# Performance work log

Measured on AMD Instinct MI355X. Metric: run time of the kernel, lower is better.

## Reference

```python
import jax, jax.numpy as jnp
import numpy as np

N_NODES = 100000
N_EDGES = 1600000
IN_CH, HID, EMB = 128, 64, 32


def _glorot(key, shape):
    lim = np.sqrt(6.0 / (shape[0] + shape[1])).astype(np.float32)
    return jax.random.uniform(key, shape, jnp.float32, -lim, lim)


def setup_inputs() -> dict:
    key = jax.random.key(0)
    ks = jax.random.split(key, 5)
    x = jax.random.normal(ks[0], (N_NODES, IN_CH), dtype=jnp.float32)
    edges = jax.random.randint(ks[1], (2, N_EDGES), 0, N_NODES)
    W1 = _glorot(ks[2], (IN_CH, HID)); b1 = jnp.zeros((HID,), jnp.float32)
    W2 = _glorot(ks[3], (HID, EMB)); b2 = jnp.zeros((EMB,), jnp.float32)
    W3 = _glorot(ks[4], (HID, EMB)); b3 = jnp.zeros((EMB,), jnp.float32)
    return {"x": x, "edges": edges, "W1": W1, "b1": b1,
            "W2": W2, "b2": b2, "W3": W3, "b3": b3}


def reference(x, edges, W1, b1, W2, b2, W3, b3):
    N = x.shape[0]
    # GCNConv default: add self-loops, symmetric D^-1/2 A D^-1/2 normalization
    loop = jnp.arange(N, dtype=edges.dtype)
    src = jnp.concatenate([edges[0], loop])  # [E+N] message sources
    dst = jnp.concatenate([edges[1], loop])  # [E+N] message targets
    deg = jax.ops.segment_sum(jnp.ones_like(dst, dtype=x.dtype), dst, num_segments=N)
    dinv = jnp.where(deg > 0, jax.lax.rsqrt(deg), 0.0)
    norm = dinv[src] * dinv[dst]  # [E+N], cached across the three convs (cached=True)

    def gcn(h, W, b):
        h = h @ W                                  # [N, out]
        msg = h[src] * norm[:, None]               # gather + edge scale
        return jax.ops.segment_sum(msg, dst, num_segments=N) + b  # scatter-add

    h = jax.nn.relu(gcn(x, W1, b1))
    return gcn(h, W2, b2), gcn(h, W3, b3)
```

## Files before the change

kernel.cpp:

```cpp
#include <hip/hip_runtime.h>

#define NN 100000
#define NE 1600000
#define NB 391
#define CHUNK 4096
#define NCHUNK 391

typedef __attribute__((ext_vector_type(8))) short short8_t;
typedef __attribute__((ext_vector_type(4))) float float4_t;

__device__ inline unsigned short f2bf(float f) {
    unsigned int u = __float_as_uint(f);
    unsigned int r = u + 0x7fffu + ((u >> 16) & 1u);
    return (unsigned short)(r >> 16);
}
__device__ inline float bf_lo(unsigned int u) { return __uint_as_float(u << 16); }
__device__ inline float bf_hi(unsigned int u) { return __uint_as_float(u & 0xffff0000u); }

__global__ __launch_bounds__(256) void k_hist(const int* __restrict__ dst,
                                              int* __restrict__ bhist) {
    __shared__ int lh[NB];
    int t = threadIdx.x;
    for (int i = t; i < NB; i += 256) lh[i] = 0;
    __syncthreads();
    for (int e = blockIdx.x * 256 + t; e < NE; e += 256 * 256)
        atomicAdd(&lh[dst[e] >> 8], 1);
    __syncthreads();
    for (int i = t; i < NB; i += 256)
        if (lh[i]) atomicAdd(&bhist[i], lh[i]);
}

__global__ __launch_bounds__(256) void k_scanb(const int* __restrict__ bhist,
                                               int* __restrict__ boff,
                                               int* __restrict__ bcur) {
    __shared__ int sh[256];
    int t = threadIdx.x;
    int base = t * 2;
    int v0 = (base + 0 < NB) ? bhist[base + 0] : 0;
    int v1 = (base + 1 < NB) ? bhist[base + 1] : 0;
    int tsum = v0 + v1;
    sh[t] = tsum;
    __syncthreads();
    for (int d = 1; d < 256; d <<= 1) {
        int x = (t >= d) ? sh[t - d] : 0;
        __syncthreads();
        sh[t] += x;
        __syncthreads();
    }
    int excl = sh[t] - tsum;
    if (base + 0 < NB) { boff[base + 0] = excl;      bcur[base + 0] = excl; }
    if (base + 1 < NB) { boff[base + 1] = excl + v0; bcur[base + 1] = excl + v0; }
    if (t == 255) boff[NB] = sh[255];
}

__global__ __launch_bounds__(512) void k_bscatter(const int* __restrict__ src,
                                                  const int* __restrict__ dst,
                                                  int* __restrict__ bcur,
                                                  unsigned int* __restrict__ pairs) {
    __shared__ int lh[NB];
    __shared__ int lbase[NB];
    int t = threadIdx.x;
    int e0 = blockIdx.x * CHUNK;
    int e1 = min(e0 + CHUNK, NE);
    for (int i = t; i < NB; i += 512) lh[i] = 0;
    __syncthreads();
    for (int e = e0 + t; e < e1; e += 512)
        atomicAdd(&lh[dst[e] >> 8], 1);
    __syncthreads();
    int rot = (int)((blockIdx.x * 97u) % NB);
    for (int i = t; i < NB; i += 512) {
        int ii = i + rot; if (ii >= NB) ii -= NB;
        int h = lh[ii];
        lbase[ii] = h ? atomicAdd(&bcur[ii], h) : 0;
    }
    __syncthreads();
    for (int i = t; i < NB; i += 512) lh[i] = 0;
    __syncthreads();
    for (int e = e0 + t; e < e1; e += 512) {
        int d = dst[e];
        int b = d >> 8;
        int r = atomicAdd(&lh[b], 1);
        pairs[lbase[b] + r] = (unsigned int)src[e] | ((unsigned int)(d & 255) << 17);
    }
}

__global__ __launch_bounds__(256) void k_fine(const unsigned int* __restrict__ pairs,
                                              const int* __restrict__ boff,
                                              int* __restrict__ csr_off,
                                              int* __restrict__ csr_src,
                                              float* __restrict__ dinv) {
    __shared__ int lcnt[256];
    __shared__ int sc[256];
    __shared__ int lofs[256];
    int t = threadIdx.x;
    int b = blockIdx.x;
    int n0 = b << 8;
    int nnode = min(256, NN - n0);
    int bO = boff[b], bE = boff[b + 1];

    lcnt[t] = 0;
    __syncthreads();
    for (int e = bO + t; e < bE; e += 256)
        atomicAdd(&lcnt[pairs[e] >> 17], 1);
    __syncthreads();
    sc[t] = lcnt[t];
    __syncthreads();
    for (int d = 1; d < 256; d <<= 1) {
        int x = (t >= d) ? sc[t - d] : 0;
        __syncthreads();
        sc[t] += x;
        __syncthreads();
    }
    {
        int excl = sc[t] - lcnt[t];
        lofs[t] = excl;
        if (t < nnode) {
            int n = n0 + t;
            csr_off[n] = bO + excl;
            dinv[n] = rsqrtf(1.0f + (float)lcnt[t]);
        }
        lcnt[t] = 0;
    }
    if (b == NB - 1 && t == 0) csr_off[NN] = NE;
    __syncthreads();
    for (int e = bO + t; e < bE; e += 256) {
        unsigned int w = pairs[e];
        int li = (int)(w >> 17);
        int r = atomicAdd(&lcnt[li], 1);
        csr_src[bO + lofs[li] + r] = (int)(w & 0x1FFFFu);
    }
}

__global__ __launch_bounds__(256) void k_w1t(const float* __restrict__ W1,
                                             unsigned short* __restrict__ wtb) {
    int f = blockIdx.x * 256 + threadIdx.x;
    int c = f >> 7, k = f & 127;
    wtb[f] = f2bf(W1[k * 64 + c]);
}

__global__ __launch_bounds__(256) void k_gemm1(const float* __restrict__ x,
                                               const unsigned short* __restrict__ wtb,
                                               const float* __restrict__ dinv,
                                               unsigned short* __restrict__ t1b) {
    __shared__ __align__(16) unsigned short lx[64 * 136];
    __shared__ __align__(16) unsigned short lw[64 * 136];
    __shared__ float sdinv[64];
    const int t = threadIdx.x;
    const int row0 = blockIdx.x * 64;
    const int nrows = min(64, NN - row0);

    #pragma unroll
    for (int i = 0; i < 8; ++i) {
        int f = t + i * 256;
        int r = f >> 5, c4 = f & 31;
        float4 v = make_float4(0.f, 0.f, 0.f, 0.f);
        if (r < nrows) v = ((const float4*)(x + (size_t)(row0 + r) * 128))[c4];
        ushort4 o;
        o.x = f2bf(v.x); o.y = f2bf(v.y); o.z = f2bf(v.z); o.w = f2bf(v.w);
        *(ushort4*)&lx[r * 136 + c4 * 4] = o;
    }
    #pragma unroll
    for (int i = 0; i < 4; ++i) {
        int f = t + i * 256;
        int c = f >> 4, c8 = f & 15;
        uint4 v = ((const uint4*)wtb)[f];
        *(uint4*)&lw[c * 136 + c8 * 8] = v;
    }
    if (t < 64) sdinv[t] = (row0 + t < NN) ? dinv[row0 + t] : 0.f;
    __syncthreads();

    const int w = t >> 6, l = t & 63;
    const int m15 = l & 15, kg = l >> 4;
    const unsigned short* pa = &lx[(w * 16 + m15) * 136 + kg * 8];
    const unsigned short* pb = &lw[m15 * 136 + kg * 8];

    float4_t acc[4];
    #pragma unroll
    for (int cb = 0; cb < 4; ++cb) acc[cb] = (float4_t){0.f, 0.f, 0.f, 0.f};

    #pragma unroll
    for (int ks = 0; ks < 4; ++ks) {
        short8_t a = *(const short8_t*)(pa + ks * 32);
        #pragma unroll
        for (int cb = 0; cb < 4; ++cb) {
            short8_t b = *(const short8_t*)(pb + cb * (16 * 136) + ks * 32);
            acc[cb] = __builtin_amdgcn_mfma_f32_16x16x32_bf16(a, b, acc[cb], 0, 0, 0);
        }
    }

    #pragma unroll
    for (int r = 0; r < 4; ++r) {
        int lrow = w * 16 + kg * 4 + r;
        if (lrow < nrows) {
            float dn = sdinv[lrow];
            size_t grow = (size_t)(row0 + lrow);
            #pragma unroll
            for (int cb = 0; cb < 4; ++cb)
                t1b[grow * 64 + cb * 16 + m15] = f2bf(acc[cb][r] * dn);
        }
    }
}

template <bool RELU>
__global__ __launch_bounds__(256) void k_gather8(const int* __restrict__ off,
                                                 const int* __restrict__ csr,
                                                 const float* __restrict__ dinv,
                                                 const unsigned short* __restrict__ hb,
                                                 const float* __restrict__ bias,
                                                 unsigned int* __restrict__ outp) {
    int idx = blockIdx.x * 256 + threadIdx.x;
    int n = idx >> 3;
    if (n >= NN) return;
    int c8 = idx & 7;
    const uint4* h4 = (const uint4*)hb;
    float dn = dinv[n];
    float acc[8];
    {
        uint4 v = h4[(size_t)n * 8 + c8];
        acc[0] = bf_lo(v.x); acc[1] = bf_hi(v.x);
        acc[2] = bf_lo(v.y); acc[3] = bf_hi(v.y);
        acc[4] = bf_lo(v.z); acc[5] = bf_hi(v.z);
        acc[6] = bf_lo(v.w); acc[7] = bf_hi(v.w);
    }
    int b = off[n], e = off[n + 1];
    int i = b;
    if (i < e) {
        int s = csr[i];
        for (++i; i < e; ++i) {
            int sn = csr[i];
            uint4 v = h4[(size_t)s * 8 + c8];
            acc[0] += bf_lo(v.x); acc[1] += bf_hi(v.x);
            acc[2] += bf_lo(v.y); acc[3] += bf_hi(v.y);
            acc[4] += bf_lo(v.z); acc[5] += bf_hi(v.z);
            acc[6] += bf_lo(v.w); acc[7] += bf_hi(v.w);
            s = sn;
        }
        uint4 v = h4[(size_t)s * 8 + c8];
        acc[0] += bf_lo(v.x); acc[1] += bf_hi(v.x);
        acc[2] += bf_lo(v.y); acc[3] += bf_hi(v.y);
        acc[4] += bf_lo(v.z); acc[5] += bf_hi(v.z);
        acc[6] += bf_lo(v.w); acc[7] += bf_hi(v.w);
    }
    float o[8];
    if (RELU) {
        float4 b0 = ((const float4*)bias)[c8 * 2];
        float4 b1 = ((const float4*)bias)[c8 * 2 + 1];
        o[0] = dn * fmaxf(dn * acc[0] + b0.x, 0.f);
        o[1] = dn * fmaxf(dn * acc[1] + b0.y, 0.f);
        o[2] = dn * fmaxf(dn * acc[2] + b0.z, 0.f);
        o[3] = dn * fmaxf(dn * acc[3] + b0.w, 0.f);
        o[4] = dn * fmaxf(dn * acc[4] + b1.x, 0.f);
        o[5] = dn * fmaxf(dn * acc[5] + b1.y, 0.f);
        o[6] = dn * fmaxf(dn * acc[6] + b1.z, 0.f);
        o[7] = dn * fmaxf(dn * acc[7] + b1.w, 0.f);
    } else {
        #pragma unroll
        for (int j = 0; j < 8; ++j) o[j] = dn * acc[j];
    }
    uint4 p;
    p.x = (unsigned int)f2bf(o[0]) | ((unsigned int)f2bf(o[1]) << 16);
    p.y = (unsigned int)f2bf(o[2]) | ((unsigned int)f2bf(o[3]) << 16);
    p.z = (unsigned int)f2bf(o[4]) | ((unsigned int)f2bf(o[5]) << 16);
    p.w = (unsigned int)f2bf(o[6]) | ((unsigned int)f2bf(o[7]) << 16);
    ((uint4*)outp)[(size_t)n * 8 + c8] = p;
}

__global__ __launch_bounds__(256) void k_gemm2(const unsigned short* __restrict__ aggb,
                                               const float* __restrict__ W2, const float* __restrict__ b2,
                                               const float* __restrict__ W3, const float* __restrict__ b3,
                                               float* __restrict__ out) {
    __shared__ float as_[64][72];
    __shared__ float wc[64 * 64];
    __shared__ float bc[64];
    const int t = threadIdx.x;
    const int row0 = blockIdx.x * 64;
    const int nrows = min(64, NN - row0);

    #pragma unroll
    for (int i = 0; i < 16; ++i) {
        int f = t + i * 256;
        int k = f >> 6, c = f & 63;
        wc[f] = (c < 32) ? W2[k * 32 + c] : W3[k * 32 + (c - 32)];
    }
    if (t < 64) bc[t] = (t < 32) ? b2[t] : b3[t - 32];
    #pragma unroll
    for (int i = 0; i < 2; ++i) {
        int f = t + i * 256;
        int r = f >> 3, c8 = f & 7;
        uint4 v = make_uint4(0u, 0u, 0u, 0u);
        if (r < nrows) v = ((const uint4*)(aggb + (size_t)(row0 + r) * 64))[c8];
        float* dp = &as_[r][c8 * 8];
        dp[0] = bf_lo(v.x); dp[1] = bf_hi(v.x);
        dp[2] = bf_lo(v.y); dp[3] = bf_hi(v.y);
        dp[4] = bf_lo(v.z); dp[5] = bf_hi(v.z);
        dp[6] = bf_lo(v.w); dp[7] = bf_hi(v.w);
    }
    __syncthreads();

    const int tc = t & 15;
    const int tr = t >> 4;
    float acc[4][4];
    #pragma unroll
    for (int i = 0; i < 4; ++i)
        #pragma unroll
        for (int j = 0; j < 4; ++j) acc[i][j] = 0.f;

    #pragma unroll 4
    for (int k = 0; k < 64; ++k) {
        float4 wv = *(const float4*)&wc[k * 64 + tc * 4];
        #pragma unroll
        for (int i = 0; i < 4; ++i) {
            float xv = as_[tr * 4 + i][k];
            acc[i][0] += xv * wv.x; acc[i][1] += xv * wv.y;
            acc[i][2] += xv * wv.z; acc[i][3] += xv * wv.w;
        }
    }
    const int c0 = tc * 4;
    float4 bias = *(float4*)&bc[c0];
    #pragma unroll
    for (int i = 0; i < 4; ++i) {
        int r = tr * 4 + i;
        if (r < nrows) {
            float4 o = make_float4(acc[i][0] + bias.x, acc[i][1] + bias.y,
                                   acc[i][2] + bias.z, acc[i][3] + bias.w);
            size_t row = (size_t)(row0 + r);
            float* p = (tc < 8) ? (out + row * 32 + c0)
                                : (out + (size_t)NN * 32 + row * 32 + (c0 - 32));
            *(float4*)p = o;
        }
    }
}

extern "C" void kernel_launch(void* const* d_in, const int* in_sizes, int n_in,
                              void* d_out, int out_size, void* d_ws, size_t ws_size,
                              hipStream_t stream) {
    const float* x  = (const float*)d_in[0];
    const int* edges = (const int*)d_in[1];
    const float* W1 = (const float*)d_in[2];
    const float* b1 = (const float*)d_in[3];
    const float* W2 = (const float*)d_in[4];
    const float* b2 = (const float*)d_in[5];
    const float* W3 = (const float*)d_in[6];
    const float* b3 = (const float*)d_in[7];
    float* out = (float*)d_out;

    const int* srcs = edges;
    const int* dsts = edges + NE;

    int*   csr_off = (int*)d_ws;
    float* dinv    = (float*)((int*)d_ws + 100004);
    int*   csr_src = (int*)d_ws + 200004;
    int*   bhist   = (int*)d_ws + 1800004;
    int*   boff    = (int*)d_ws + 1800396;
    int*   bcur    = (int*)d_ws + 1800788;
    unsigned short* wtb = (unsigned short*)((int*)d_ws + 1801184);
    unsigned int*   pairs = (unsigned int*)((int*)d_ws + 1805280);
    unsigned short* t1b   = (unsigned short*)pairs;
    unsigned short* aggb  = (unsigned short*)pairs;
    unsigned short* h1b   = (unsigned short*)((int*)d_ws + 5005280);

    dim3 blk(256);
    const int gN8 = (NN * 8 + 255) / 256;
    const int gT = (NN + 63) / 64;

    hipMemsetAsync(bhist, 0, NB * sizeof(int), stream);
    k_hist<<<256, blk, 0, stream>>>(dsts, bhist);
    k_w1t<<<32, blk, 0, stream>>>(W1, wtb);
    k_scanb<<<1, blk, 0, stream>>>(bhist, boff, bcur);
    k_bscatter<<<NCHUNK, dim3(512), 0, stream>>>(srcs, dsts, bcur, pairs);
    k_fine<<<NB, blk, 0, stream>>>(pairs, boff, csr_off, csr_src, dinv);

    k_gemm1<<<gT, blk, 0, stream>>>(x, wtb, dinv, t1b);
    k_gather8<true><<<gN8, blk, 0, stream>>>(csr_off, csr_src, dinv, t1b, b1,
                                             (unsigned int*)h1b);
    k_gather8<false><<<gN8, blk, 0, stream>>>(csr_off, csr_src, dinv, h1b, b1,
                                              (unsigned int*)aggb);
    k_gemm2<<<gT, blk, 0, stream>>>(aggb, W2, b2, W3, b3, out);
}
```

Baseline: 162.4 us.

## Fuse second-layer gather into the final GEMM and enlarge GEMM1 tiles

The second aggregation pass (gather over CSR neighbours of h1) is folded into the final W2/W3 GEMM kernel. Each block gathers its 64 rows straight into shared memory, so the bf16 aggregate buffer is never written and re-read and one launch is dropped. Each thread now handles 16 channels (4 threads per node) with a one-ahead index prefetch, which gives less parallelism per node than the old 8-thread gather and may hurt latency hiding. Separately, GEMM1 moves to 128-row tiles with 512 threads, so there are fewer blocks and W1 is loaded fewer times.

```diff
diff --git a/kernel.cpp b/kernel.cpp
--- a/kernel.cpp
+++ b/kernel.cpp
@@ -138,20 +138,20 @@
     wtb[f] = f2bf(W1[k * 64 + c]);
 }
 
-__global__ __launch_bounds__(256) void k_gemm1(const float* __restrict__ x,
+__global__ __launch_bounds__(512) void k_gemm1(const float* __restrict__ x,
                                                const unsigned short* __restrict__ wtb,
                                                const float* __restrict__ dinv,
                                                unsigned short* __restrict__ t1b) {
-    __shared__ __align__(16) unsigned short lx[64 * 136];
+    __shared__ __align__(16) unsigned short lx[128 * 136];
     __shared__ __align__(16) unsigned short lw[64 * 136];
-    __shared__ float sdinv[64];
+    __shared__ float sdinv[128];
     const int t = threadIdx.x;
-    const int row0 = blockIdx.x * 64;
-    const int nrows = min(64, NN - row0);
+    const int row0 = blockIdx.x * 128;
+    const int nrows = min(128, NN - row0);
 
     #pragma unroll
     for (int i = 0; i < 8; ++i) {
-        int f = t + i * 256;
+        int f = t + i * 512;
         int r = f >> 5, c4 = f & 31;
         float4 v = make_float4(0.f, 0.f, 0.f, 0.f);
         if (r < nrows) v = ((const float4*)(x + (size_t)(row0 + r) * 128))[c4];
@@ -160,13 +160,13 @@
         *(ushort4*)&lx[r * 136 + c4 * 4] = o;
     }
     #pragma unroll
-    for (int i = 0; i < 4; ++i) {
-        int f = t + i * 256;
+    for (int i = 0; i < 2; ++i) {
+        int f = t + i * 512;
         int c = f >> 4, c8 = f & 15;
         uint4 v = ((const uint4*)wtb)[f];
         *(uint4*)&lw[c * 136 + c8 * 8] = v;
     }
-    if (t < 64) sdinv[t] = (row0 + t < NN) ? dinv[row0 + t] : 0.f;
+    if (t < 128) sdinv[t] = (row0 + t < NN) ? dinv[row0 + t] : 0.f;
     __syncthreads();
 
     const int w = t >> 6, l = t & 63;
@@ -265,10 +265,13 @@
     ((uint4*)outp)[(size_t)n * 8 + c8] = p;
 }
 
-__global__ __launch_bounds__(256) void k_gemm2(const unsigned short* __restrict__ aggb,
-                                               const float* __restrict__ W2, const float* __restrict__ b2,
-                                               const float* __restrict__ W3, const float* __restrict__ b3,
-                                               float* __restrict__ out) {
+__global__ __launch_bounds__(256) void k_gg2(const int* __restrict__ off,
+                                             const int* __restrict__ csr,
+                                             const float* __restrict__ dinv,
+                                             const unsigned short* __restrict__ hb,
+                                             const float* __restrict__ W2, const float* __restrict__ b2,
+                                             const float* __restrict__ W3, const float* __restrict__ b3,
+                                             float* __restrict__ out) {
     __shared__ float as_[64][72];
     __shared__ float wc[64 * 64];
     __shared__ float bc[64];
@@ -283,17 +286,63 @@
         wc[f] = (c < 32) ? W2[k * 32 + c] : W3[k * 32 + (c - 32)];
     }
     if (t < 64) bc[t] = (t < 32) ? b2[t] : b3[t - 32];
-    #pragma unroll
-    for (int i = 0; i < 2; ++i) {
-        int f = t + i * 256;
-        int r = f >> 3, c8 = f & 7;
-        uint4 v = make_uint4(0u, 0u, 0u, 0u);
-        if (r < nrows) v = ((const uint4*)(aggb + (size_t)(row0 + r) * 64))[c8];
-        float* dp = &as_[r][c8 * 8];
-        dp[0] = bf_lo(v.x); dp[1] = bf_hi(v.x);
-        dp[2] = bf_lo(v.y); dp[3] = bf_hi(v.y);
-        dp[4] = bf_lo(v.z); dp[5] = bf_hi(v.z);
-        dp[6] = bf_lo(v.w); dp[7] = bf_hi(v.w);
+
+    {
+        const int nl = t >> 2;
+        const int n = row0 + nl;
+        const int c16 = t & 3;
+        float acc[16];
+        if (n < NN) {
+            const uint4* h4 = (const uint4*)hb;
+            float dn = dinv[n];
+            size_t base = (size_t)n * 8 + c16 * 2;
+            uint4 v0 = h4[base], v1 = h4[base + 1];
+            acc[0]  = bf_lo(v0.x); acc[1]  = bf_hi(v0.x);
+            acc[2]  = bf_lo(v0.y); acc[3]  = bf_hi(v0.y);
+            acc[4]  = bf_lo(v0.z); acc[5]  = bf_hi(v0.z);
+            acc[6]  = bf_lo(v0.w); acc[7]  = bf_hi(v0.w);
+            acc[8]  = bf_lo(v1.x); acc[9]  = bf_hi(v1.x);
+            acc[10] = bf_lo(v1.y); acc[11] = bf_hi(v1.y);
+            acc[12] = bf_lo(v1.z); acc[13] = bf_hi(v1.z);
+            acc[14] = bf_lo(v1.w); acc[15] = bf_hi(v1.w);
+            int b = off[n], e = off[n + 1];
+            int i = b;
+            if (i < e) {
+                int s = csr[i];
+                for (++i; i < e; ++i) {
+                    int sn = csr[i];
+                    size_t sb = (size_t)s * 8 + c16 * 2;
+                    uint4 w0 = h4[sb], w1 = h4[sb + 1];
+                    acc[0]  += bf_lo(w0.x); acc[1]  += bf_hi(w0.x);
+                    acc[2]  += bf_lo(w0.y); acc[3]  += bf_hi(w0.y);
+                    acc[4]  += bf_lo(w0.z); acc[5]  += bf_hi(w0.z);
+                    acc[6]  += bf_lo(w0.w); acc[7]  += bf_hi(w0.w);
+                    acc[8]  += bf_lo(w1.x); acc[9]  += bf_hi(w1.x);
+                    acc[10] += bf_lo(w1.y); acc[11] += bf_hi(w1.y);
+                    acc[12] += bf_lo(w1.z); acc[13] += bf_hi(w1.z);
+                    acc[14] += bf_lo(w1.w); acc[15] += bf_hi(w1.w);
+                    s = sn;
+                }
+                size_t sb = (size_t)s * 8 + c16 * 2;
+                uint4 w0 = h4[sb], w1 = h4[sb + 1];
+                acc[0]  += bf_lo(w0.x); acc[1]  += bf_hi(w0.x);
+                acc[2]  += bf_lo(w0.y); acc[3]  += bf_hi(w0.y);
+                acc[4]  += bf_lo(w0.z); acc[5]  += bf_hi(w0.z);
+                acc[6]  += bf_lo(w0.w); acc[7]  += bf_hi(w0.w);
+                acc[8]  += bf_lo(w1.x); acc[9]  += bf_hi(w1.x);
+                acc[10] += bf_lo(w1.y); acc[11] += bf_hi(w1.y);
+                acc[12] += bf_lo(w1.z); acc[13] += bf_hi(w1.z);
+                acc[14] += bf_lo(w1.w); acc[15] += bf_hi(w1.w);
+            }
+            #pragma unroll
+            for (int j = 0; j < 16; ++j) acc[j] *= dn;
+        } else {
+            #pragma unroll
+            for (int j = 0; j < 16; ++j) acc[j] = 0.f;
+        }
+        float* dp = &as_[nl][c16 * 16];
+        #pragma unroll
+        for (int j = 0; j < 16; ++j) dp[j] = acc[j];
     }
     __syncthreads();
 
@@ -356,12 +405,12 @@
     unsigned short* wtb = (unsigned short*)((int*)d_ws + 1801184);
     unsigned int*   pairs = (unsigned int*)((int*)d_ws + 1805280);
     unsigned short* t1b   = (unsigned short*)pairs;
-    unsigned short* aggb  = (unsigned short*)pairs;
     unsigned short* h1b   = (unsigned short*)((int*)d_ws + 5005280);
 
     dim3 blk(256);
     const int gN8 = (NN * 8 + 255) / 256;
-    const int gT = (NN + 63) / 64;
+    const int gT  = (NN + 63) / 64;
+    const int gT1 = (NN + 127) / 128;
 
     hipMemsetAsync(bhist, 0, NB * sizeof(int), stream);
     k_hist<<<256, blk, 0, stream>>>(dsts, bhist);
@@ -370,10 +419,8 @@
     k_bscatter<<<NCHUNK, dim3(512), 0, stream>>>(srcs, dsts, bcur, pairs);
     k_fine<<<NB, blk, 0, stream>>>(pairs, boff, csr_off, csr_src, dinv);
 
-    k_gemm1<<<gT, blk, 0, stream>>>(x, wtb, dinv, t1b);
+    k_gemm1<<<gT1, dim3(512), 0, stream>>>(x, wtb, dinv, t1b);
     k_gather8<true><<<gN8, blk, 0, stream>>>(csr_off, csr_src, dinv, t1b, b1,
                                              (unsigned int*)h1b);
-    k_gather8<false><<<gN8, blk, 0, stream>>>(csr_off, csr_src, dinv, h1b, b1,
-                                              (unsigned int*)aggb);
-    k_gemm2<<<gT, blk, 0, stream>>>(aggb, W2, b2, W3, b3, out);
-}
+    k_gg2<<<gT, blk, 0, stream>>>(csr_off, csr_src, dinv, h1b, W2, b2, W3, b3, out);
+}
```

Result: faster. 158.4 us (-2.5%).
